# Kernel optimization log

Measured on AMD Instinct MI355X. Metric: run time of the kernel, lower is better.

## Reference

```python
import jax, jax.numpy as jnp
import numpy as np

V, D, H, L, F, B, S = 512, 512, 8, 6, 2048, 8, 1024
DK = D // H
EPS = 1e-5


def _positional_encoding(max_len, d_model):
    pos = np.arange(max_len, dtype=np.float32)[:, None]
    div = np.exp(np.arange(0, d_model, 2, dtype=np.float32) * (-np.log(10000.0) / d_model))
    pe = np.zeros((max_len, d_model), dtype=np.float32)
    pe[:, 0::2] = np.sin(pos * div)
    pe[:, 1::2] = np.cos(pos * div)
    return jnp.asarray(pe)


def setup_inputs() -> dict:
    key = jax.random.key(0)
    ks = jax.random.split(key, 24)
    xavier = lambda k, shp: jax.random.normal(k, shp, jnp.float32) * np.sqrt(2.0 / (shp[-2] + shp[-1]))
    inp = {
        "input_ids": jax.random.randint(ks[0], (B, S), 0, V),
        "emb": jax.random.normal(ks[1], (V, D), jnp.float32) * 0.02,
        "pe": _positional_encoding(1024, D),
        "Wq": xavier(ks[2], (L, D, D)), "bq": jnp.zeros((L, D)),
        "Wk": xavier(ks[3], (L, D, D)), "bk": jnp.zeros((L, D)),
        "Wv": xavier(ks[4], (L, D, D)), "bv": jnp.zeros((L, D)),
        "Wo": xavier(ks[5], (L, D, D)), "bo": jnp.zeros((L, D)),
        "ln1_g": jnp.ones((L, D)), "ln1_b": jnp.zeros((L, D)),
        "W1": xavier(ks[6], (L, D, F)), "b1": jnp.zeros((L, F)),
        "W2": xavier(ks[7], (L, F, D)), "b2": jnp.zeros((L, D)),
        "ln2_g": jnp.ones((L, D)), "ln2_b": jnp.zeros((L, D)),
        "Wout": xavier(ks[8], (D, V)), "bout": jnp.zeros((V,)),
    }
    return inp


def _ln(x, g, b):
    mu = jnp.mean(x, -1, keepdims=True)
    var = jnp.mean(jnp.square(x - mu), -1, keepdims=True)
    return (x - mu) * jax.lax.rsqrt(var + EPS) * g + b


def reference(input_ids, emb, pe, Wq, bq, Wk, bk, Wv, bv, Wo, bo,
              ln1_g, ln1_b, W1, b1, W2, b2, ln2_g, ln2_b, Wout, bout):
    h = emb[input_ids] * np.sqrt(D) + pe[:S]  # [B,S,D]
    # Faithful to the original mask bug: masked_fill(mask==0, -1e9) fills the
    # LOWER triangle (incl diagonal); raw scores are kept strictly where j > i.
    r = jnp.arange(S)
    keep = r[None, :] > r[:, None]  # [S,S]

    def block(h, p):
        (wq, bq_, wk, bk_, wv, bv_, wo, bo_,
         g1, be1, w1, b1_, w2, b2_, g2, be2) = p
        split = lambda t: t.reshape(B, S, H, DK).transpose(0, 2, 1, 3)
        q = split(h @ wq + bq_)
        k = split(h @ wk + bk_)
        v = split(h @ wv + bv_)
        scores = jnp.einsum('bhqd,bhkd->bhqk', q, k) / np.sqrt(DK)
        scores = jnp.where(keep, scores, -1e9)
        a = jax.nn.softmax(scores, axis=-1)
        o = jnp.einsum('bhqk,bhkd->bhqd', a, v).transpose(0, 2, 1, 3).reshape(B, S, D)
        h = _ln(h + (o @ wo + bo_), g1, be1)
        f = jax.nn.relu(h @ w1 + b1_) @ w2 + b2_
        h = _ln(h + f, g2, be2)
        return h, None

    params = (Wq, bq, Wk, bk, Wv, bv, Wo, bo, ln1_g, ln1_b, W1, b1, W2, b2, ln2_g, ln2_b)
    h, _ = jax.lax.scan(block, h, params)
    return h @ Wout + bout  # logits [B,S,V]
```

## Files before the change

kernel.cpp:

```cpp
#include <hip/hip_runtime.h>

typedef unsigned short u16;
typedef __attribute__((ext_vector_type(8))) short bf16x8;
typedef __attribute__((ext_vector_type(4))) float f32x4;
typedef __attribute__((ext_vector_type(4))) unsigned int uint4v;
typedef __attribute__((ext_vector_type(4))) unsigned short us4;

#define NLAYER 6
#define D_MODEL 512
#define NHEAD 8
#define DKH 64
#define SEQ 1024
#define BATCH 8
#define FFN 2048
#define MROWS (BATCH * SEQ)
#define QKV_LD 1536
#define SCALE_LOG2E 0.18033688011112042f

__device__ __forceinline__ float b2f(u16 u) {
  union { unsigned u32; float f; } x; x.u32 = ((unsigned)u) << 16; return x.f;
}
__device__ __forceinline__ u16 f2b(float f) {
  union { float f; unsigned u; } x; x.f = f;
  unsigned r = x.u + 0x7FFFu + ((x.u >> 16) & 1u);
  return (u16)(r >> 16);
}
__device__ __forceinline__ void gld16(const u16* g, u16* l) {
  __builtin_amdgcn_global_load_lds(
      (const __attribute__((address_space(1))) unsigned int*)g,
      (__attribute__((address_space(3))) unsigned int*)l, 16, 0, 0);
}
__device__ __forceinline__ void barrier_raw() {
  asm volatile("" ::: "memory");
  __builtin_amdgcn_s_barrier();
  asm volatile("" ::: "memory");
}

__global__ __launch_bounds__(256) void transpose_cvt_kernel(
    const float* __restrict__ src, u16* __restrict__ dst, int K, int N, size_t dstZ,
    float scale)
{
  __shared__ float t[32][33];
  const int z = blockIdx.z;
  src += (size_t)z * K * N;
  dst += (size_t)z * dstZ;
  const int n0 = blockIdx.x * 32, k0 = blockIdx.y * 32;
  const int tx = threadIdx.x, ty = threadIdx.y;
#pragma unroll
  for (int i = 0; i < 32; i += 8)
    t[ty + i][tx] = src[(size_t)(k0 + ty + i) * N + n0 + tx];
  __syncthreads();
#pragma unroll
  for (int i = 0; i < 32; i += 8)
    dst[(size_t)(n0 + ty + i) * K + k0 + tx] = f2b(t[tx][ty + i] * scale);
}

__global__ __launch_bounds__(256) void concat_bias_kernel(
    const float* __restrict__ bq, const float* __restrict__ bk,
    const float* __restrict__ bv, float* __restrict__ dst)
{
  const int l = blockIdx.x, t = threadIdx.x;
#pragma unroll
  for (int j = t; j < 512; j += 256) {
    dst[l * QKV_LD + j]        = bq[l * 512 + j] * SCALE_LOG2E;
    dst[l * QKV_LD + 512 + j]  = bk[l * 512 + j];
    dst[l * QKV_LD + 1024 + j] = bv[l * 512 + j];
  }
}

__global__ __launch_bounds__(256) void embed_kernel(
    const int* __restrict__ ids, const float* __restrict__ emb,
    const float* __restrict__ pe, float* __restrict__ Hf, u16* __restrict__ Hb)
{
  const int row = blockIdx.x;
  const int s = row & (SEQ - 1);
  const int id = ids[row];
  const int tid = threadIdx.x;
#pragma unroll
  for (int u = 0; u < 2; ++u) {
    const int d = tid + u * 256;
    float v = emb[(size_t)id * D_MODEL + d] * 22.62741699796952f + pe[(size_t)s * D_MODEL + d];
    Hf[(size_t)row * D_MODEL + d] = v;
    Hb[(size_t)row * D_MODEL + d] = f2b(v);
  }
}

template<bool RELU, bool VT>
__global__ __launch_bounds__(512, 2) void gemm256_kernel(
    const u16* __restrict__ A, const u16* __restrict__ Bt,
    const float* __restrict__ bias,
    u16* __restrict__ Cb, u16* __restrict__ Vtp,
    int M, int N, int K)
{
  extern __shared__ __align__(16) u16 smem[];
  u16* Asm = smem;
  u16* Bsm = smem + 32768;
  const int tid = threadIdx.x;
  const int wave = tid >> 6, lane = tid & 63;
  const int lm = lane & 15, quad = lane >> 4, l7 = lm & 7;
  const int wm = wave >> 2, wn = wave & 3;
  const int bm = blockIdx.x * 256, bn = blockIdx.y * 256;

  const int srow = tid >> 3;
  const int scg = (tid & 7) ^ (srow & 7);
  const u16* Ap = A  + (size_t)(bm + srow) * K + scg * 8;
  const u16* Bp = Bt + (size_t)(bn + srow) * K + scg * 8;
  u16* uA = Asm + wave * 512;
  u16* uB = Bsm + wave * 512;

  f32x4 acc[8][4] = {};

  const int NT = K >> 6;
  auto stage = [&](int buf, int t) {
    const size_t ko = (size_t)t << 6;
#pragma unroll
    for (int p = 0; p < 4; ++p)
      gld16(Ap + (size_t)(p * 64) * K + ko, uA + buf * 16384 + p * 4096);
#pragma unroll
    for (int p = 0; p < 4; ++p)
      gld16(Bp + (size_t)(p * 64) * K + ko, uB + buf * 16384 + p * 4096);
  };

  stage(0, 0);
  __syncthreads();

  const int sl0 = (quad ^ l7) << 3;
  const int sl1 = ((quad + 4) ^ l7) << 3;

#pragma unroll 1
  for (int t = 0; t < NT; ++t) {
    const int cur = t & 1;
    if (t + 1 < NT) stage(cur ^ 1, t + 1);
    const u16* as_ = Asm + cur * 16384 + (wm * 128 + lm) * 64;
    const u16* bs_ = Bsm + cur * 16384 + (wn * 64 + lm) * 64;
    bf16x8 af[4][2], b01[2][2], b23[2][2];
#pragma unroll
    for (int i = 0; i < 4; ++i) {
      af[i][0] = *(const bf16x8*)&as_[i * 1024 + sl0];
      af[i][1] = *(const bf16x8*)&as_[i * 1024 + sl1];
    }
#pragma unroll
    for (int j = 0; j < 2; ++j) {
      b01[j][0] = *(const bf16x8*)&bs_[j * 1024 + sl0];
      b01[j][1] = *(const bf16x8*)&bs_[j * 1024 + sl1];
    }
    __builtin_amdgcn_s_setprio(1);
#pragma unroll
    for (int i = 0; i < 4; ++i)
#pragma unroll
      for (int j = 0; j < 2; ++j) {
        acc[i][j] = __builtin_amdgcn_mfma_f32_16x16x32_bf16(af[i][0], b01[j][0], acc[i][j], 0, 0, 0);
        acc[i][j] = __builtin_amdgcn_mfma_f32_16x16x32_bf16(af[i][1], b01[j][1], acc[i][j], 0, 0, 0);
      }
    __builtin_amdgcn_s_setprio(0);
    barrier_raw();
#pragma unroll
    for (int j = 0; j < 2; ++j) {
      b23[j][0] = *(const bf16x8*)&bs_[(j + 2) * 1024 + sl0];
      b23[j][1] = *(const bf16x8*)&bs_[(j + 2) * 1024 + sl1];
    }
    __builtin_amdgcn_s_setprio(1);
#pragma unroll
    for (int i = 0; i < 4; ++i)
#pragma unroll
      for (int j = 0; j < 2; ++j) {
        acc[i][j + 2] = __builtin_amdgcn_mfma_f32_16x16x32_bf16(af[i][0], b23[j][0], acc[i][j + 2], 0, 0, 0);
        acc[i][j + 2] = __builtin_amdgcn_mfma_f32_16x16x32_bf16(af[i][1], b23[j][1], acc[i][j + 2], 0, 0, 0);
      }
    __builtin_amdgcn_s_setprio(0);
    barrier_raw();
#pragma unroll
    for (int i = 0; i < 4; ++i) {
      af[i][0] = *(const bf16x8*)&as_[(i + 4) * 1024 + sl0];
      af[i][1] = *(const bf16x8*)&as_[(i + 4) * 1024 + sl1];
    }
    __builtin_amdgcn_s_setprio(1);
#pragma unroll
    for (int i = 0; i < 4; ++i)
#pragma unroll
      for (int j = 0; j < 2; ++j) {
        acc[i + 4][j + 2] = __builtin_amdgcn_mfma_f32_16x16x32_bf16(af[i][0], b23[j][0], acc[i + 4][j + 2], 0, 0, 0);
        acc[i + 4][j + 2] = __builtin_amdgcn_mfma_f32_16x16x32_bf16(af[i][1], b23[j][1], acc[i + 4][j + 2], 0, 0, 0);
      }
    __builtin_amdgcn_s_setprio(0);
    barrier_raw();
#pragma unroll
    for (int j = 0; j < 2; ++j) {
      b01[j][0] = *(const bf16x8*)&bs_[j * 1024 + sl0];
      b01[j][1] = *(const bf16x8*)&bs_[j * 1024 + sl1];
    }
    __builtin_amdgcn_s_setprio(1);
#pragma unroll
    for (int i = 0; i < 4; ++i)
#pragma unroll
      for (int j = 0; j < 2; ++j) {
        acc[i + 4][j] = __builtin_amdgcn_mfma_f32_16x16x32_bf16(af[i][0], b01[j][0], acc[i + 4][j], 0, 0, 0);
        acc[i + 4][j] = __builtin_amdgcn_mfma_f32_16x16x32_bf16(af[i][1], b01[j][1], acc[i + 4][j], 0, 0, 0);
      }
    __builtin_amdgcn_s_setprio(0);
    if (t + 1 < NT) {
      asm volatile("s_waitcnt vmcnt(0)" ::: "memory");
      barrier_raw();
    }
  }

  const int mbase = bm + wm * 128 + quad * 4;
  const int nbase = bn + wn * 64 + lm;
#pragma unroll
  for (int i = 0; i < 8; ++i) {
#pragma unroll
    for (int j = 0; j < 4; ++j) {
      const int n = nbase + j * 16;
      const float bv = bias[n];
      float vv[4];
#pragma unroll
      for (int r = 0; r < 4; ++r) {
        float v = acc[i][j][r] + bv;
        if (RELU) v = fmaxf(v, 0.f);
        vv[r] = v;
      }
      if (VT && n >= 1024) {
        const int hh = (n - 1024) >> 6, d = (n - 1024) & 63;
        const int mm = mbase + i * 16;
        const int bb = mm >> 10, ss = mm & 1023;
        us4 pk;
#pragma unroll
        for (int r = 0; r < 4; ++r) pk[r] = f2b(vv[r]);
        *(us4*)&Vtp[(((size_t)(bb * NHEAD + hh)) * 64 + d) * SEQ + ss] = pk;
      } else {
#pragma unroll
        for (int r = 0; r < 4; ++r) {
          const int m = mbase + i * 16 + r;
          Cb[(size_t)m * N + n] = f2b(vv[r]);
        }
      }
    }
  }
}

template<bool LN>
__global__ __launch_bounds__(512, 2) void gemm_ln_kernel(
    const u16* __restrict__ A, const u16* __restrict__ Bt,
    const float* __restrict__ bias,
    const float* __restrict__ gw, const float* __restrict__ bw,
    float* __restrict__ Hf, u16* __restrict__ Hb, float* __restrict__ Cf,
    int K)
{
  extern __shared__ __align__(16) u16 smem[];
  u16* Asm = smem;
  u16* Bsm = smem + 8192;
  float* red = (float*)(smem + 73728);
  const int tid = threadIdx.x;
  const int wave = tid >> 6, lane = tid & 63;
  const int lm = lane & 15, quad = lane >> 4, l7 = lm & 7;
  const int bm = blockIdx.x * 64;

  const int srow = tid >> 3;
  const int scg = (tid & 7) ^ (srow & 7);
  const u16* Ap = A  + (size_t)(bm + srow) * K + scg * 8;
  const u16* Bp = Bt + (size_t)srow * K + scg * 8;

  f32x4 acc[4][4] = {};
  const int NT = K >> 6;
  auto stage = [&](int buf, int t) {
    const size_t ko = (size_t)t << 6;
    gld16(Ap + ko, Asm + buf * 4096 + wave * 512);
#pragma unroll
    for (int p = 0; p < 8; ++p)
      gld16(Bp + (size_t)(p * 64) * K + ko, Bsm + buf * 32768 + p * 4096 + wave * 512);
  };

  stage(0, 0);
  __syncthreads();

#pragma unroll 1
  for (int t = 0; t < NT; ++t) {
    const int cur = t & 1;
    if (t + 1 < NT) stage(cur ^ 1, t + 1);
    const u16* as_ = Asm + cur * 4096 + lm * 64;
    const u16* bs_ = Bsm + cur * 32768 + (wave * 64 + lm) * 64;
#pragma unroll
    for (int kh = 0; kh < 2; ++kh) {
      const int slot = ((kh * 4 + quad) ^ l7) << 3;
      bf16x8 af[4], bg[4];
#pragma unroll
      for (int i = 0; i < 4; ++i)
        af[i] = *(const bf16x8*)&as_[i * 1024 + slot];
#pragma unroll
      for (int j = 0; j < 4; ++j)
        bg[j] = *(const bf16x8*)&bs_[j * 1024 + slot];
#pragma unroll
      for (int i = 0; i < 4; ++i)
#pragma unroll
        for (int j = 0; j < 4; ++j)
          acc[i][j] = __builtin_amdgcn_mfma_f32_16x16x32_bf16(af[i], bg[j], acc[i][j], 0, 0, 0);
    }
    __syncthreads();
  }

  const int col0 = wave * 64 + lm;
  float bi[4];
#pragma unroll
  for (int j = 0; j < 4; ++j) bi[j] = bias[col0 + j * 16];

  if (LN) {
    float gv[4], bv[4];
#pragma unroll
    for (int j = 0; j < 4; ++j) { gv[j] = gw[col0 + j * 16]; bv[j] = bw[col0 + j * 16]; }
    float x[4][4][4];
    float ps[16], pq[16];
#pragma unroll
    for (int k = 0; k < 16; ++k) { ps[k] = 0.f; pq[k] = 0.f; }
#pragma unroll
    for (int i = 0; i < 4; ++i)
#pragma unroll
      for (int r = 0; r < 4; ++r) {
        const int rowl = i * 16 + quad * 4 + r;
        const size_t rb = (size_t)(bm + rowl) * D_MODEL;
#pragma unroll
        for (int j = 0; j < 4; ++j) {
          float xv = acc[i][j][r] + bi[j] + Hf[rb + col0 + j * 16];
          x[i][j][r] = xv;
          ps[i * 4 + r] += xv;
          pq[i * 4 + r] += xv * xv;
        }
      }
#pragma unroll
    for (int o = 1; o < 16; o <<= 1)
#pragma unroll
      for (int k = 0; k < 16; ++k) {
        ps[k] += __shfl_xor(ps[k], o, 16);
        pq[k] += __shfl_xor(pq[k], o, 16);
      }
    if (lm == 0) {
#pragma unroll
      for (int k = 0; k < 16; ++k) {
        const int rowl = (k >> 2) * 16 + quad * 4 + (k & 3);
        red[wave * 64 + rowl] = ps[k];
        red[512 + wave * 64 + rowl] = pq[k];
      }
    }
    __syncthreads();
    if (tid < 64) {
      float s = 0.f, q = 0.f;
#pragma unroll
      for (int w = 0; w < 8; ++w) { s += red[w * 64 + tid]; q += red[512 + w * 64 + tid]; }
      const float mu = s * (1.f / 512.f);
      const float var = q * (1.f / 512.f) - mu * mu;
      red[1024 + tid] = mu;
      red[1088 + tid] = rsqrtf(var + 1e-5f);
    }
    __syncthreads();
#pragma unroll
    for (int i = 0; i < 4; ++i)
#pragma unroll
      for (int r = 0; r < 4; ++r) {
        const int rowl = i * 16 + quad * 4 + r;
        const float mu = red[1024 + rowl];
        const float rs = red[1088 + rowl];
        const size_t rb = (size_t)(bm + rowl) * D_MODEL;
#pragma unroll
        for (int j = 0; j < 4; ++j) {
          const float y = (x[i][j][r] - mu) * rs * gv[j] + bv[j];
          Hf[rb + col0 + j * 16] = y;
          Hb[rb + col0 + j * 16] = f2b(y);
        }
      }
  } else {
#pragma unroll
    for (int i = 0; i < 4; ++i)
#pragma unroll
      for (int r = 0; r < 4; ++r) {
        const int rowl = i * 16 + quad * 4 + r;
        const size_t rb = (size_t)(bm + rowl) * D_MODEL;
#pragma unroll
        for (int j = 0; j < 4; ++j)
          Cf[rb + col0 + j * 16] = acc[i][j][r] + bi[j];
      }
  }
}

__global__ __launch_bounds__(256) void attn_mfma_kernel(
    const u16* __restrict__ QKV, const u16* __restrict__ Vt, u16* __restrict__ O)
{
  __shared__ __align__(16) u16 Ks[64 * 64];
  __shared__ __align__(16) u16 Vs[64 * 64];
  __shared__ __align__(16) u16 Ps[4 * 16 * 64];
  const int tid = threadIdx.x;
  const int wave = tid >> 6, lane = tid & 63;
  const int quad = lane >> 4, l15 = lane & 15;
  const int l7 = l15 & 7;
  const int id = blockIdx.x;
  const int bh = id & 63;
  const int b = bh >> 3, h = bh & 7;
  const int g = id >> 6;
  const int u = g * 4 + wave;
  u16* psw = Ps + wave * (16 * 64);
  const size_t qoff = (size_t)b * SEQ * QKV_LD + h * 64;
  const size_t vtb  = (size_t)bh * 64 * SEQ;

  const int sr = tid >> 3, sc = tid & 7;
  const u16* kg0 = QKV + qoff + 512 + (size_t)sr * QKV_LD + sc * 8;
  const u16* kg1 = kg0 + (size_t)32 * QKV_LD;
  const u16* vg0 = Vt + vtb + (size_t)sr * SEQ + sc * 8;
  const u16* vg1 = vg0 + (size_t)32 * SEQ;
  const int sw = (sc ^ (sr & 7)) << 3;
  u16* ks0 = &Ks[sr * 64 + sw];
  u16* ks1 = &Ks[(sr + 32) * 64 + sw];
  u16* vs0 = &Vs[sr * 64 + sw];
  u16* vs1 = &Vs[(sr + 32) * 64 + sw];

  const u16* qp = QKV + qoff + (size_t)(u * 16 + l15) * QKV_LD + quad * 8;
  const bf16x8 qf0 = *(const bf16x8*)(qp);
  const bf16x8 qf1 = *(const bf16x8*)(qp + 32);

  f32x4 oacc[4] = {};
  float lsum[4] = {0.f, 0.f, 0.f, 0.f};

  uint4v kr0 = *(const uint4v*)(kg0 + (size_t)(g * 64) * QKV_LD);
  uint4v kr1 = *(const uint4v*)(kg1 + (size_t)(g * 64) * QKV_LD);
  uint4v vr0 = *(const uint4v*)(vg0 + g * 64);
  uint4v vr1 = *(const uint4v*)(vg1 + g * 64);

#pragma unroll 1
  for (int jt = g; jt < 16; ++jt) {
    __syncthreads();
    *(uint4v*)ks0 = kr0; *(uint4v*)ks1 = kr1;
    *(uint4v*)vs0 = vr0; *(uint4v*)vs1 = vr1;
    __syncthreads();
    if (jt < 15) {
      kr0 = *(const uint4v*)(kg0 + (size_t)((jt + 1) * 64) * QKV_LD);
      kr1 = *(const uint4v*)(kg1 + (size_t)((jt + 1) * 64) * QKV_LD);
      vr0 = *(const uint4v*)(vg0 + (jt + 1) * 64);
      vr1 = *(const uint4v*)(vg1 + (jt + 1) * 64);
    }
    f32x4 sacc[4] = {};
#pragma unroll
    for (int nt = 0; nt < 4; ++nt) {
      const int key = nt * 16 + l15, k7 = key & 7;
      bf16x8 kb0 = *(const bf16x8*)&Ks[key * 64 + ((quad ^ k7) << 3)];
      bf16x8 kb1 = *(const bf16x8*)&Ks[key * 64 + (((quad + 4) ^ k7) << 3)];
      sacc[nt] = __builtin_amdgcn_mfma_f32_16x16x32_bf16(qf0, kb0, sacc[nt], 0, 0, 0);
      sacc[nt] = __builtin_amdgcn_mfma_f32_16x16x32_bf16(qf1, kb1, sacc[nt], 0, 0, 0);
    }
    const bool diag = (jt == g);
#pragma unroll
    for (int nt = 0; nt < 4; ++nt)
#pragma unroll
      for (int r = 0; r < 4; ++r) {
        float pv = __builtin_amdgcn_exp2f(sacc[nt][r]);
        if (diag) {
          const int i = u * 16 + quad * 4 + r;
          const int j = jt * 64 + nt * 16 + l15;
          pv = (j > i) ? pv : 0.f;
        }
        lsum[r] += pv;
        const int qr = quad * 4 + r;
        const int j2 = nt * 16 + l15;
        psw[qr * 64 + (((j2 >> 3) ^ (qr & 7)) << 3) + (j2 & 7)] = f2b(pv);
      }
    bf16x8 pf0 = *(const bf16x8*)&psw[l15 * 64 + (((quad + 0) ^ l7) << 3)];
    bf16x8 pf1 = *(const bf16x8*)&psw[l15 * 64 + (((quad + 4) ^ l7) << 3)];
#pragma unroll
    for (int nt = 0; nt < 4; ++nt) {
      const int d = nt * 16 + l15, d7 = d & 7;
      bf16x8 vb0 = *(const bf16x8*)&Vs[d * 64 + ((quad ^ d7) << 3)];
      bf16x8 vb1 = *(const bf16x8*)&Vs[d * 64 + (((quad + 4) ^ d7) << 3)];
      oacc[nt] = __builtin_amdgcn_mfma_f32_16x16x32_bf16(pf0, vb0, oacc[nt], 0, 0, 0);
      oacc[nt] = __builtin_amdgcn_mfma_f32_16x16x32_bf16(pf1, vb1, oacc[nt], 0, 0, 0);
    }
  }

#pragma unroll
  for (int o = 1; o < 16; o <<= 1)
#pragma unroll
    for (int r = 0; r < 4; ++r) lsum[r] += __shfl_xor(lsum[r], o, 16);
  float rl[4];
#pragma unroll
  for (int r = 0; r < 4; ++r) rl[r] = 1.0f / lsum[r];
#pragma unroll
  for (int nt = 0; nt < 4; ++nt)
#pragma unroll
    for (int r = 0; r < 4; ++r) {
      const int row = u * 16 + quad * 4 + r;
      O[(size_t)(b * SEQ + row) * D_MODEL + h * DKH + nt * 16 + l15] = f2b(oacc[nt][r] * rl[r]);
    }

  if (g == 15) {
    __syncthreads();
    const int d = tid >> 2, scv = (tid & 3) * 256;
    const u16* pv = Vt + vtb + (size_t)d * SEQ + scv;
    float s = 0.f;
#pragma unroll 8
    for (int i2 = 0; i2 < 256; ++i2) s += b2f(pv[i2]);
    s += __shfl_xor(s, 1, 64);
    s += __shfl_xor(s, 2, 64);
    if ((tid & 3) == 0)
      O[((size_t)b * SEQ + SEQ - 1) * D_MODEL + h * 64 + d] = f2b(s * (1.f / SEQ));
  }
}

extern "C" void kernel_launch(void* const* d_in, const int* in_sizes, int n_in,
                              void* d_out, int out_size, void* d_ws, size_t ws_size,
                              hipStream_t stream) {
  (void)in_sizes; (void)n_in; (void)out_size; (void)ws_size;
  const int*   ids  = (const int*)  d_in[0];
  const float* emb  = (const float*)d_in[1];
  const float* pe   = (const float*)d_in[2];
  const float* Wq   = (const float*)d_in[3];
  const float* bq   = (const float*)d_in[4];
  const float* Wk   = (const float*)d_in[5];
  const float* bk   = (const float*)d_in[6];
  const float* Wv   = (const float*)d_in[7];
  const float* bv   = (const float*)d_in[8];
  const float* Wo   = (const float*)d_in[9];
  const float* bo   = (const float*)d_in[10];
  const float* g1   = (const float*)d_in[11];
  const float* be1  = (const float*)d_in[12];
  const float* W1   = (const float*)d_in[13];
  const float* b1   = (const float*)d_in[14];
  const float* W2   = (const float*)d_in[15];
  const float* b2   = (const float*)d_in[16];
  const float* g2   = (const float*)d_in[17];
  const float* be2  = (const float*)d_in[18];
  const float* Wout = (const float*)d_in[19];
  const float* bout = (const float*)d_in[20];
  float* out = (float*)d_out;

  static int attr_set = 0;
  if (!attr_set) {
    hipFuncSetAttribute(reinterpret_cast<const void*>(&gemm256_kernel<false, true>),
                        hipFuncAttributeMaxDynamicSharedMemorySize, 131072);
    hipFuncSetAttribute(reinterpret_cast<const void*>(&gemm256_kernel<true, false>),
                        hipFuncAttributeMaxDynamicSharedMemorySize, 131072);
    hipFuncSetAttribute(reinterpret_cast<const void*>(&gemm_ln_kernel<true>),
                        hipFuncAttributeMaxDynamicSharedMemorySize, 152064);
    hipFuncSetAttribute(reinterpret_cast<const void*>(&gemm_ln_kernel<false>),
                        hipFuncAttributeMaxDynamicSharedMemorySize, 152064);
    attr_set = 1;
  }

  char* wsp = (char*)d_ws;
  auto alloc = [&](size_t bytes) -> char* {
    char* p = wsp; wsp += (bytes + 255) & ~(size_t)255; return p;
  };
  const size_t dd  = (size_t)D_MODEL * D_MODEL;
  const size_t df  = (size_t)D_MODEL * FFN;
  const size_t dq  = (size_t)QKV_LD * D_MODEL;
  u16* wqkv_t = (u16*)alloc(NLAYER * dq * 2);
  u16* wo_t   = (u16*)alloc(NLAYER * dd * 2);
  u16* w1_t   = (u16*)alloc(NLAYER * df * 2);
  u16* w2_t   = (u16*)alloc(NLAYER * df * 2);
  u16* wout_t = (u16*)alloc(dd * 2);
  float* bqkv = (float*)alloc(NLAYER * QKV_LD * 4);
  float* hf   = (float*)alloc((size_t)MROWS * D_MODEL * 4);
  u16*   hb   = (u16*)  alloc((size_t)MROWS * D_MODEL * 2);
  u16*   qkvb = (u16*)  alloc((size_t)MROWS * QKV_LD * 2);
  u16*   ob   = (u16*)  alloc((size_t)MROWS * D_MODEL * 2);
  u16*   vt   = (u16*)  alloc((size_t)BATCH * NHEAD * DKH * SEQ * 2);
  u16*   mid  = qkvb;

  dim3 tb8(32, 8);
  transpose_cvt_kernel<<<dim3(16, 16, NLAYER), tb8, 0, stream>>>(Wq, wqkv_t,            512, 512,  dq, SCALE_LOG2E);
  transpose_cvt_kernel<<<dim3(16, 16, NLAYER), tb8, 0, stream>>>(Wk, wqkv_t + 512*512,  512, 512,  dq, 1.f);
  transpose_cvt_kernel<<<dim3(16, 16, NLAYER), tb8, 0, stream>>>(Wv, wqkv_t + 1024*512, 512, 512,  dq, 1.f);
  transpose_cvt_kernel<<<dim3(16, 16, NLAYER), tb8, 0, stream>>>(Wo, wo_t,   512, 512,  dd, 1.f);
  transpose_cvt_kernel<<<dim3(64, 16, NLAYER), tb8, 0, stream>>>(W1, w1_t,   512, 2048, df, 1.f);
  transpose_cvt_kernel<<<dim3(16, 64, NLAYER), tb8, 0, stream>>>(W2, w2_t,   2048, 512, df, 1.f);
  transpose_cvt_kernel<<<dim3(16, 16, 1),      tb8, 0, stream>>>(Wout, wout_t, 512, 512, dd, 1.f);
  concat_bias_kernel<<<NLAYER, 256, 0, stream>>>(bq, bk, bv, bqkv);

  embed_kernel<<<MROWS, 256, 0, stream>>>(ids, emb, pe, hf, hb);

  for (int l = 0; l < NLAYER; ++l) {
    gemm256_kernel<false, true><<<dim3(32, 6), 512, 131072, stream>>>(
        hb, wqkv_t + l * dq, bqkv + l * QKV_LD, qkvb, vt, MROWS, QKV_LD, 512);
    attn_mfma_kernel<<<1024, 256, 0, stream>>>(qkvb, vt, ob);
    gemm_ln_kernel<true><<<128, 512, 152064, stream>>>(
        ob, wo_t + l * dd, bo + l * 512, g1 + l * 512, be1 + l * 512,
        hf, hb, nullptr, 512);
    gemm256_kernel<true, false><<<dim3(32, 8), 512, 131072, stream>>>(
        hb, w1_t + l * df, b1 + l * 2048, mid, nullptr, MROWS, 2048, 512);
    gemm_ln_kernel<true><<<128, 512, 152064, stream>>>(
        mid, w2_t + l * df, b2 + l * 512, g2 + l * 512, be2 + l * 512,
        hf, hb, nullptr, 2048);
  }
  gemm_ln_kernel<false><<<128, 512, 152064, stream>>>(
      hb, wout_t, bout, nullptr, nullptr, nullptr, nullptr, out, 512);
}
```

Baseline: 1.003 ms.

## Register-staged prefetch in gemm_ln kernel and use 32-row tiles for K=512 GEMMs

Replaces the global_load_lds double-buffered staging in the fused GEMM+LayerNorm kernel with loads into registers two tiles ahead, followed by explicit LDS writes and raw barriers. This deepens the prefetch pipeline. The kernel is also templated on the row-tile size, and the Wo and output-projection GEMMs (K=512) use 32-row tiles with 256 blocks to fill more CUs. The costs are higher register pressure from the B0/B1 staging arrays, more barriers per iteration, and half the MFMA reuse of B per block for the BM=32 variant.

```diff
diff --git a/kernel.cpp b/kernel.cpp
--- a/kernel.cpp
+++ b/kernel.cpp
@@ -34,6 +34,9 @@
   asm volatile("" ::: "memory");
   __builtin_amdgcn_s_barrier();
   asm volatile("" ::: "memory");
+}
+__device__ __forceinline__ void lgkm0() {
+  asm volatile("s_waitcnt lgkmcnt(0)" ::: "memory");
 }
 
 __global__ __launch_bounds__(256) void transpose_cvt_kernel(
@@ -238,7 +241,7 @@
   }
 }
 
-template<bool LN>
+template<int BM, bool LN>
 __global__ __launch_bounds__(512, 2) void gemm_ln_kernel(
     const u16* __restrict__ A, const u16* __restrict__ Bt,
     const float* __restrict__ bias,
@@ -246,56 +249,85 @@
     float* __restrict__ Hf, u16* __restrict__ Hb, float* __restrict__ Cf,
     int K)
 {
+  constexpr int IT = BM / 16;
   extern __shared__ __align__(16) u16 smem[];
   u16* Asm = smem;
-  u16* Bsm = smem + 8192;
-  float* red = (float*)(smem + 73728);
+  u16* Bsm = smem + 2 * BM * 64;
+  float* red = (float*)(smem + 2 * BM * 64 + 65536);
   const int tid = threadIdx.x;
   const int wave = tid >> 6, lane = tid & 63;
   const int lm = lane & 15, quad = lane >> 4, l7 = lm & 7;
-  const int bm = blockIdx.x * 64;
+  const int bm = blockIdx.x * BM;
 
   const int srow = tid >> 3;
   const int scg = (tid & 7) ^ (srow & 7);
-  const u16* Ap = A  + (size_t)(bm + srow) * K + scg * 8;
+  const bool doA = (BM == 64) || (wave < 4);
+  const u16* Ap = A  + (size_t)(bm + (doA ? srow : 0)) * K + scg * 8;
   const u16* Bp = Bt + (size_t)srow * K + scg * 8;
-
-  f32x4 acc[4][4] = {};
+  u16* wB = Bsm + wave * 512 + (lane << 3);
+  u16* wA = Asm + wave * 512 + (lane << 3);
+
+  f32x4 acc[IT][4] = {};
   const int NT = K >> 6;
-  auto stage = [&](int buf, int t) {
+
+  uint4v B0[8], B1[8], A0, A1;
+  auto loadr = [&](uint4v (&rB)[8], uint4v& rA, int t) {
     const size_t ko = (size_t)t << 6;
-    gld16(Ap + ko, Asm + buf * 4096 + wave * 512);
 #pragma unroll
     for (int p = 0; p < 8; ++p)
-      gld16(Bp + (size_t)(p * 64) * K + ko, Bsm + buf * 32768 + p * 4096 + wave * 512);
+      rB[p] = *(const uint4v*)(Bp + (size_t)(p * 64) * K + ko);
+    if (doA) rA = *(const uint4v*)(Ap + ko);
   };
-
-  stage(0, 0);
-  __syncthreads();
-
-#pragma unroll 1
-  for (int t = 0; t < NT; ++t) {
-    const int cur = t & 1;
-    if (t + 1 < NT) stage(cur ^ 1, t + 1);
-    const u16* as_ = Asm + cur * 4096 + lm * 64;
-    const u16* bs_ = Bsm + cur * 32768 + (wave * 64 + lm) * 64;
+  auto writes = [&](uint4v (&rB)[8], uint4v& rA, int buf) {
+#pragma unroll
+    for (int p = 0; p < 8; ++p)
+      *(uint4v*)(wB + buf * 32768 + p * 4096) = rB[p];
+    if (doA) *(uint4v*)(wA + buf * (BM * 64)) = rA;
+  };
+  auto compute = [&](int buf) {
+    const u16* as_ = Asm + buf * (BM * 64) + lm * 64;
+    const u16* bs_ = Bsm + buf * 32768 + (wave * 64 + lm) * 64;
 #pragma unroll
     for (int kh = 0; kh < 2; ++kh) {
       const int slot = ((kh * 4 + quad) ^ l7) << 3;
-      bf16x8 af[4], bg[4];
-#pragma unroll
-      for (int i = 0; i < 4; ++i)
+      bf16x8 af[IT], bg[4];
+#pragma unroll
+      for (int i = 0; i < IT; ++i)
         af[i] = *(const bf16x8*)&as_[i * 1024 + slot];
 #pragma unroll
       for (int j = 0; j < 4; ++j)
         bg[j] = *(const bf16x8*)&bs_[j * 1024 + slot];
 #pragma unroll
-      for (int i = 0; i < 4; ++i)
+      for (int i = 0; i < IT; ++i)
 #pragma unroll
         for (int j = 0; j < 4; ++j)
           acc[i][j] = __builtin_amdgcn_mfma_f32_16x16x32_bf16(af[i], bg[j], acc[i][j], 0, 0, 0);
     }
-    __syncthreads();
+  };
+
+  loadr(B0, A0, 0);
+  writes(B0, A0, 0);
+  loadr(B0, A0, 1);
+  loadr(B1, A1, 2);
+  lgkm0();
+  barrier_raw();
+
+#pragma unroll 1
+  for (int t = 0; t < NT; t += 2) {
+    compute(0);
+    barrier_raw();
+    writes(B0, A0, 1);
+    if (t + 3 < NT) loadr(B0, A0, t + 3);
+    lgkm0();
+    barrier_raw();
+    compute(1);
+    barrier_raw();
+    if (t + 2 < NT) {
+      writes(B1, A1, 0);
+      if (t + 4 < NT) loadr(B1, A1, t + 4);
+    }
+    lgkm0();
+    barrier_raw();
   }
 
   const int col0 = wave * 64 + lm;
@@ -307,12 +339,12 @@
     float gv[4], bv[4];
 #pragma unroll
     for (int j = 0; j < 4; ++j) { gv[j] = gw[col0 + j * 16]; bv[j] = bw[col0 + j * 16]; }
-    float x[4][4][4];
-    float ps[16], pq[16];
-#pragma unroll
-    for (int k = 0; k < 16; ++k) { ps[k] = 0.f; pq[k] = 0.f; }
-#pragma unroll
-    for (int i = 0; i < 4; ++i)
+    float x[IT][4][4];
+    float ps[IT * 4], pq[IT * 4];
+#pragma unroll
+    for (int k = 0; k < IT * 4; ++k) { ps[k] = 0.f; pq[k] = 0.f; }
+#pragma unroll
+    for (int i = 0; i < IT; ++i)
 #pragma unroll
       for (int r = 0; r < 4; ++r) {
         const int rowl = i * 16 + quad * 4 + r;
@@ -328,36 +360,36 @@
 #pragma unroll
     for (int o = 1; o < 16; o <<= 1)
 #pragma unroll
-      for (int k = 0; k < 16; ++k) {
+      for (int k = 0; k < IT * 4; ++k) {
         ps[k] += __shfl_xor(ps[k], o, 16);
         pq[k] += __shfl_xor(pq[k], o, 16);
       }
     if (lm == 0) {
 #pragma unroll
-      for (int k = 0; k < 16; ++k) {
+      for (int k = 0; k < IT * 4; ++k) {
         const int rowl = (k >> 2) * 16 + quad * 4 + (k & 3);
-        red[wave * 64 + rowl] = ps[k];
-        red[512 + wave * 64 + rowl] = pq[k];
+        red[wave * BM + rowl] = ps[k];
+        red[8 * BM + wave * BM + rowl] = pq[k];
       }
     }
     __syncthreads();
-    if (tid < 64) {
+    if (tid < BM) {
       float s = 0.f, q = 0.f;
 #pragma unroll
-      for (int w = 0; w < 8; ++w) { s += red[w * 64 + tid]; q += red[512 + w * 64 + tid]; }
+      for (int w = 0; w < 8; ++w) { s += red[w * BM + tid]; q += red[8 * BM + w * BM + tid]; }
       const float mu = s * (1.f / 512.f);
       const float var = q * (1.f / 512.f) - mu * mu;
-      red[1024 + tid] = mu;
-      red[1088 + tid] = rsqrtf(var + 1e-5f);
+      red[16 * BM + tid] = mu;
+      red[17 * BM + tid] = rsqrtf(var + 1e-5f);
     }
     __syncthreads();
 #pragma unroll
-    for (int i = 0; i < 4; ++i)
+    for (int i = 0; i < IT; ++i)
 #pragma unroll
       for (int r = 0; r < 4; ++r) {
         const int rowl = i * 16 + quad * 4 + r;
-        const float mu = red[1024 + rowl];
-        const float rs = red[1088 + rowl];
+        const float mu = red[16 * BM + rowl];
+        const float rs = red[17 * BM + rowl];
         const size_t rb = (size_t)(bm + rowl) * D_MODEL;
 #pragma unroll
         for (int j = 0; j < 4; ++j) {
@@ -368,7 +400,7 @@
       }
   } else {
 #pragma unroll
-    for (int i = 0; i < 4; ++i)
+    for (int i = 0; i < IT; ++i)
 #pragma unroll
       for (int r = 0; r < 4; ++r) {
         const int rowl = i * 16 + quad * 4 + r;
@@ -533,10 +565,12 @@
                         hipFuncAttributeMaxDynamicSharedMemorySize, 131072);
     hipFuncSetAttribute(reinterpret_cast<const void*>(&gemm256_kernel<true, false>),
                         hipFuncAttributeMaxDynamicSharedMemorySize, 131072);
-    hipFuncSetAttribute(reinterpret_cast<const void*>(&gemm_ln_kernel<true>),
+    hipFuncSetAttribute(reinterpret_cast<const void*>(&gemm_ln_kernel<64, true>),
                         hipFuncAttributeMaxDynamicSharedMemorySize, 152064);
-    hipFuncSetAttribute(reinterpret_cast<const void*>(&gemm_ln_kernel<false>),
-                        hipFuncAttributeMaxDynamicSharedMemorySize, 152064);
+    hipFuncSetAttribute(reinterpret_cast<const void*>(&gemm_ln_kernel<32, true>),
+                        hipFuncAttributeMaxDynamicSharedMemorySize, 141568);
+    hipFuncSetAttribute(reinterpret_cast<const void*>(&gemm_ln_kernel<32, false>),
+                        hipFuncAttributeMaxDynamicSharedMemorySize, 141568);
     attr_set = 1;
   }
 
@@ -576,15 +610,15 @@
     gemm256_kernel<false, true><<<dim3(32, 6), 512, 131072, stream>>>(
         hb, wqkv_t + l * dq, bqkv + l * QKV_LD, qkvb, vt, MROWS, QKV_LD, 512);
     attn_mfma_kernel<<<1024, 256, 0, stream>>>(qkvb, vt, ob);
-    gemm_ln_kernel<true><<<128, 512, 152064, stream>>>(
+    gemm_ln_kernel<32, true><<<256, 512, 141568, stream>>>(
         ob, wo_t + l * dd, bo + l * 512, g1 + l * 512, be1 + l * 512,
         hf, hb, nullptr, 512);
     gemm256_kernel<true, false><<<dim3(32, 8), 512, 131072, stream>>>(
         hb, w1_t + l * df, b1 + l * 2048, mid, nullptr, MROWS, 2048, 512);
-    gemm_ln_kernel<true><<<128, 512, 152064, stream>>>(
+    gemm_ln_kernel<64, true><<<128, 512, 152064, stream>>>(
         mid, w2_t + l * df, b2 + l * 512, g2 + l * 512, be2 + l * 512,
         hf, hb, nullptr, 2048);
   }
-  gemm_ln_kernel<false><<<128, 512, 152064, stream>>>(
+  gemm_ln_kernel<32, false><<<256, 512, 141568, stream>>>(
       hb, wout_t, bout, nullptr, nullptr, nullptr, nullptr, out, 512);
 }
```

Result: slower. 1.035 ms (+3.2%).
